# Performance work log

Hardware: AMD Instinct MI355X
Metric: run time of the kernel (lower is better)

Reference implementation:

```python
import jax, jax.numpy as jnp
import numpy as np

N = 500000      # examples = M * (nr+1)
K = 20          # context set size (indices[:, 3:])
NR = 24         # negatives per positive
H = 128         # hidden_channels == node feature dim
NODES = 10000   # ingredient vocabulary


def setup_inputs() -> dict:
    key = jax.random.key(0)
    ks = jax.random.split(key, 6)
    indices = jax.random.randint(ks[0], (N, 3 + K), 0, NODES)
    x = jax.random.normal(ks[1], (NODES, H), dtype=jnp.float32)
    scale = 0.02
    W1 = jax.random.normal(ks[2], (H, 3 * H), dtype=jnp.float32) * scale
    b1 = jnp.zeros((H,), jnp.float32)
    W2 = jax.random.normal(ks[3], (H // 2, H), dtype=jnp.float32) * scale
    b2 = jnp.zeros((H // 2,), jnp.float32)
    W3 = jax.random.normal(ks[4], (1, H // 2), dtype=jnp.float32) * scale
    b3 = jnp.zeros((1,), jnp.float32)
    return {"indices": indices, "nr": NR, "x": x,
            "W1": W1, "b1": b1, "W2": W2, "b2": b2, "W3": W3, "b3": b3}


def _embed_context(ctx_idx, x, nr):
    # ctx_idx: [N, K]; one context row per group of (nr+1) examples
    new_idx = ctx_idx[:-1:nr + 1]                 # [M, K]
    emb = x[new_idx]                               # [M, K, H] gather
    s = emb.sum(axis=1)                            # [M, H]
    norm = jnp.maximum((new_idx > 0).sum(axis=1), 1).astype(x.dtype)[:, None]
    mean = s / norm                                # masked mean over context
    return jnp.repeat(mean, nr + 1, axis=0)        # broadcast back to [N, H]


def reference(indices, nr, x, W1, b1, W2, b2, W3, b3):
    ing1 = x[indices[:, 0]]                        # [N, H]
    ing2 = x[indices[:, 1]]                        # [N, H]
    set_emb = _embed_context(indices[:, 3:], x, nr)  # [N, H]
    y = jnp.concatenate([ing1, ing2, set_emb], axis=1)  # [N, 3H]
    y = jax.nn.relu(y @ W1.T + b1)
    y = jax.nn.relu(y @ W2.T + b2)
    return y @ W3.T + b3                           # [N, 1]
```

## Files before the change

kernel.cpp:

```cpp
#include <hip/hip_runtime.h>
#include <hip/hip_bf16.h>

#define N_ROWS   500000
#define NR1      25
#define NGROUPS  20000
#define KCTX     20
#define H        128
#define NODES    10000
#define IDX_COLS 23

#define NT       4
#define RPB      (NT * 128)
#define MAXG     22

typedef __attribute__((ext_vector_type(8))) short short8;
typedef __attribute__((ext_vector_type(4))) float f32x4;

__device__ __forceinline__ unsigned pkbf(float lo, float hi) {
  __hip_bfloat162 h = __float22bfloat162_rn(make_float2(lo, hi));
  union { __hip_bfloat162 h; unsigned u; } c; c.h = h;
  return c.u;
}
__device__ __forceinline__ float bf2f(unsigned short u) {
  union { unsigned u; float f; } c; c.u = ((unsigned)u) << 16; return c.f;
}

#define PN 64
#define PRE_BLOCKS ((NODES + PN - 1) / PN)
__global__ __launch_bounds__(256) void k_precompute(
    const float* __restrict__ x, const float* __restrict__ W1,
    const int* __restrict__ indices,
    unsigned short* __restrict__ Pb, int2* __restrict__ idx2) {
  const int tid = threadIdx.x;
  const int m   = blockIdx.y;

  if (m == 3) {
    const int stride = PRE_BLOCKS * 256;
    for (int r = blockIdx.x * 256 + tid; r < N_ROWS; r += stride) {
      idx2[r] = make_int2(indices[(size_t)r * IDX_COLS + 0],
                          indices[(size_t)r * IDX_COLS + 1]);
    }
    return;
  }

  __shared__ short wlds[128][136];
  const int tbase = blockIdx.x * PN;

#pragma unroll
  for (int it = 0; it < 16; ++it) {
    const int f  = it * 256 + tid;
    const int j  = f >> 5;
    const int q4 = f & 31;
    const float4 v = *(const float4*)(W1 + (size_t)j * (3 * H) + m * H + q4 * 4);
    *(unsigned*)&wlds[j][q4 * 4]     = pkbf(v.x, v.y);
    *(unsigned*)&wlds[j][q4 * 4 + 2] = pkbf(v.z, v.w);
  }
  __syncthreads();

  const int lane = tid & 63;
  const int wv   = tid >> 6;
  const int col  = lane & 15;
  const int quad = lane >> 4;

  int node = tbase + wv * 16 + col;
  if (node > NODES - 1) node = NODES - 1;
  const float4* __restrict__ xr = (const float4*)(x + (size_t)node * H);

  short8 Af[4];
#pragma unroll
  for (int kt = 0; kt < 4; ++kt) {
    const int f4 = kt * 8 + quad * 2;
    const float4 v0 = xr[f4], v1 = xr[f4 + 1];
    union { short8 v; unsigned u[4]; } pk;
    pk.u[0] = pkbf(v0.x, v0.y);
    pk.u[1] = pkbf(v0.z, v0.w);
    pk.u[2] = pkbf(v1.x, v1.y);
    pk.u[3] = pkbf(v1.z, v1.w);
    Af[kt] = pk.v;
  }

  f32x4 acc[8];
#pragma unroll
  for (int ct = 0; ct < 8; ++ct) acc[ct] = (f32x4)(0.f);

#pragma unroll
  for (int kt = 0; kt < 4; ++kt) {
#pragma unroll
    for (int ct = 0; ct < 8; ++ct) {
      const short8 Bf = *(const short8*)&wlds[ct * 16 + col][kt * 32 + quad * 8];
      acc[ct] = __builtin_amdgcn_mfma_f32_16x16x32_bf16(Af[kt], Bf, acc[ct], 0, 0, 0);
    }
  }

  unsigned short* __restrict__ Pm = Pb + (size_t)m * NODES * H;
#pragma unroll
  for (int reg = 0; reg < 4; ++reg) {
    const int n = tbase + wv * 16 + quad * 4 + reg;
    if (n < NODES) {
#pragma unroll
      for (int ct = 0; ct < 8; ++ct) {
        union { unsigned u; unsigned short s[2]; } c;
        c.u = pkbf(acc[ct][reg], 0.f);
        Pm[(size_t)n * H + ct * 16 + col] = c.s[0];
      }
    }
  }
}

__global__ __launch_bounds__(256) void k_main(
    const int* __restrict__ indices, const int2* __restrict__ idx2,
    const unsigned short* __restrict__ P1b, const unsigned short* __restrict__ P2b,
    const unsigned short* __restrict__ P3b,
    const float* __restrict__ W2, const float* __restrict__ b1,
    const float* __restrict__ b2, const float* __restrict__ W3,
    const float* __restrict__ b3, float* __restrict__ out) {
  __shared__ short w2s[64][136];
  __shared__ float cgs[MAXG][132];

  const int tid   = threadIdx.x;
  const int rbase = blockIdx.x * RPB;
  const int gbase = rbase / NR1;

  for (int idx = tid; idx < 64 * 64; idx += 256) {
    const int n  = idx >> 6;
    const int kp = idx & 63;
    const float2 w = *(const float2*)(W2 + (size_t)n * H + kp * 2);
    *(unsigned*)&w2s[n][kp * 2] = pkbf(w.x, w.y);
  }

  {
    int rlast = rbase + RPB - 1; if (rlast > N_ROWS - 1) rlast = N_ROWS - 1;
    const int G   = rlast / NR1 - gbase + 1;
    const int jj  = (tid & 63) * 2;
    const int sub = tid >> 6;
    const float2 b1v = *(const float2*)(b1 + jj);
#pragma unroll
    for (int it = 0; it < 6; ++it) {
      const int gi = it * 4 + sub;
      if (gi < G) {
        const int* __restrict__ rowidx =
            indices + (size_t)(gbase + gi) * NR1 * IDX_COLS + 3;
        float s0 = 0.f, s1 = 0.f;
        int cnt = 0;
#pragma unroll
        for (int c = 0; c < KCTX; ++c) {
          const int idx = rowidx[c];
          const unsigned w = *(const unsigned*)(P3b + (size_t)idx * H + jj);
          s0 += bf2f((unsigned short)(w & 0xffffu));
          s1 += bf2f((unsigned short)(w >> 16));
          cnt += (idx > 0) ? 1 : 0;
        }
        const float rn = 1.f / (float)((cnt > 1) ? cnt : 1);
        cgs[gi][jj]     = b1v.x + s0 * rn;
        cgs[gi][jj + 1] = b1v.y + s1 * rn;
      }
    }
  }
  __syncthreads();

  const int lane = tid & 63;
  const int wv   = tid >> 6;
  const int col  = lane & 15;
  const int quad = lane >> 4;

  float b2v[4], w3v[4];
#pragma unroll
  for (int ct = 0; ct < 4; ++ct) {
    b2v[ct] = b2[ct * 16 + col];
    w3v[ct] = W3[ct * 16 + col];
  }
  const float bias3 = b3[0];

  short8 ua[2][2][4], ub[2][2][4];
  int    gl[2][2];

  {
    const int R = rbase + wv * 32;
#pragma unroll
    for (int rt = 0; rt < 2; ++rt) {
      const int r  = R + rt * 16 + col;
      const int rc = (r < N_ROWS) ? r : (N_ROWS - 1);
      const int2 ii = idx2[rc];
      const short8* __restrict__ pa = (const short8*)(P1b + (size_t)ii.x * H);
      const short8* __restrict__ pb = (const short8*)(P2b + (size_t)ii.y * H);
#pragma unroll
      for (int kt = 0; kt < 4; ++kt) {
        ua[0][rt][kt] = pa[kt * 4 + quad];
        ub[0][rt][kt] = pb[kt * 4 + quad];
      }
      gl[0][rt] = rc / NR1 - gbase;
    }
  }

#pragma unroll
  for (int t = 0; t < NT; ++t) {
    const int cur = t & 1;
    const int nxt = cur ^ 1;
    const int Rt  = rbase + t * 128 + wv * 32;

    short8 A[2][4];
#pragma unroll
    for (int rt = 0; rt < 2; ++rt) {
#pragma unroll
      for (int kt = 0; kt < 4; ++kt) {
        union { short8 v; unsigned short s[8]; } va, vb;
        va.v = ua[cur][rt][kt];
        vb.v = ub[cur][rt][kt];
        const float4 c0 = *(const float4*)&cgs[gl[cur][rt]][kt * 32 + quad * 8];
        const float4 c1 = *(const float4*)&cgs[gl[cur][rt]][kt * 32 + quad * 8 + 4];
        const float h0 = fmaxf(bf2f(va.s[0]) + bf2f(vb.s[0]) + c0.x, 0.f);
        const float h1 = fmaxf(bf2f(va.s[1]) + bf2f(vb.s[1]) + c0.y, 0.f);
        const float h2 = fmaxf(bf2f(va.s[2]) + bf2f(vb.s[2]) + c0.z, 0.f);
        const float h3 = fmaxf(bf2f(va.s[3]) + bf2f(vb.s[3]) + c0.w, 0.f);
        const float h4 = fmaxf(bf2f(va.s[4]) + bf2f(vb.s[4]) + c1.x, 0.f);
        const float h5 = fmaxf(bf2f(va.s[5]) + bf2f(vb.s[5]) + c1.y, 0.f);
        const float h6 = fmaxf(bf2f(va.s[6]) + bf2f(vb.s[6]) + c1.z, 0.f);
        const float h7 = fmaxf(bf2f(va.s[7]) + bf2f(vb.s[7]) + c1.w, 0.f);
        union { short8 v; unsigned u[4]; } pk;
        pk.u[0] = pkbf(h0, h1);
        pk.u[1] = pkbf(h2, h3);
        pk.u[2] = pkbf(h4, h5);
        pk.u[3] = pkbf(h6, h7);
        A[rt][kt] = pk.v;
      }
    }

    if (t + 1 < NT) {
      const int Rn = rbase + (t + 1) * 128 + wv * 32;
#pragma unroll
      for (int rt = 0; rt < 2; ++rt) {
        const int r  = Rn + rt * 16 + col;
        const int rc = (r < N_ROWS) ? r : (N_ROWS - 1);
        const int2 ii = idx2[rc];
        const short8* __restrict__ pa = (const short8*)(P1b + (size_t)ii.x * H);
        const short8* __restrict__ pb = (const short8*)(P2b + (size_t)ii.y * H);
#pragma unroll
        for (int kt = 0; kt < 4; ++kt) {
          ua[nxt][rt][kt] = pa[kt * 4 + quad];
          ub[nxt][rt][kt] = pb[kt * 4 + quad];
        }
        gl[nxt][rt] = rc / NR1 - gbase;
      }
    }

    f32x4 acc[2][4];
#pragma unroll
    for (int rt = 0; rt < 2; ++rt)
#pragma unroll
      for (int ct = 0; ct < 4; ++ct) acc[rt][ct] = (f32x4)(0.f);
#pragma unroll
    for (int kt = 0; kt < 4; ++kt) {
#pragma unroll
      for (int ct = 0; ct < 4; ++ct) {
        const short8 Bf = *(const short8*)&w2s[ct * 16 + col][kt * 32 + quad * 8];
#pragma unroll
        for (int rt = 0; rt < 2; ++rt)
          acc[rt][ct] = __builtin_amdgcn_mfma_f32_16x16x32_bf16(
              A[rt][kt], Bf, acc[rt][ct], 0, 0, 0);
      }
    }
#pragma unroll
    for (int rt = 0; rt < 2; ++rt) {
#pragma unroll
      for (int reg = 0; reg < 4; ++reg) {
        float s = 0.f;
#pragma unroll
        for (int ct = 0; ct < 4; ++ct)
          s += fmaxf(acc[rt][ct][reg] + b2v[ct], 0.f) * w3v[ct];
        s += __shfl_xor(s, 1);
        s += __shfl_xor(s, 2);
        s += __shfl_xor(s, 4);
        s += __shfl_xor(s, 8);
        if (col == 0) {
          const int row = Rt + rt * 16 + quad * 4 + reg;
          if (row < N_ROWS) out[row] = s + bias3;
        }
      }
    }
  }
}

extern "C" void kernel_launch(void* const* d_in, const int* in_sizes, int n_in,
                              void* d_out, int out_size, void* d_ws, size_t ws_size,
                              hipStream_t stream) {
  const int*   indices = (const int*)  d_in[0];
  const float* x  = (const float*)d_in[2];
  const float* W1 = (const float*)d_in[3];
  const float* b1 = (const float*)d_in[4];
  const float* W2 = (const float*)d_in[5];
  const float* b2 = (const float*)d_in[6];
  const float* W3 = (const float*)d_in[7];
  const float* b3 = (const float*)d_in[8];
  float* out = (float*)d_out;

  unsigned short* Pb  = (unsigned short*)d_ws;
  unsigned short* P1b = Pb;
  unsigned short* P2b = Pb + (size_t)NODES * H;
  unsigned short* P3b = Pb + (size_t)2 * NODES * H;
  int2* idx2 = (int2*)(Pb + (size_t)3 * NODES * H);

  dim3 gpre(PRE_BLOCKS, 4);
  k_precompute<<<gpre, 256, 0, stream>>>(x, W1, indices, Pb, idx2);
  k_main<<<(N_ROWS + RPB - 1) / RPB, 256, 0, stream>>>(indices, idx2,
                                                       P1b, P2b, P3b,
                                                       W2, b1, b2, W3, b3, out);
}
```

Before: 158.4 us.

## Process 128 rows per block and issue gathers before shared setup

Each block now handles a single 128-row tile instead of four, which removes the in-block double-buffered prefetch loop and launches four times as many blocks. The gathers of the first-layer partial rows are issued at the very start of the kernel, so their latency overlaps the W2 staging and the context-group reduction into shared memory. The cost is that every block repeats the W2 conversion to shared memory, and each block has fewer groups to amortise the context sums over, so redundant context work at tile boundaries goes up.

Measured after the change: 170.1 us. 7.4% more time.

```diff
diff --git a/kernel.cpp b/kernel.cpp
--- a/kernel.cpp
+++ b/kernel.cpp
@@ -9,9 +9,8 @@
 #define NODES    10000
 #define IDX_COLS 23
 
-#define NT       4
-#define RPB      (NT * 128)
-#define MAXG     22
+#define RPB      128
+#define MAXG     7
 
 typedef __attribute__((ext_vector_type(8))) short short8;
 typedef __attribute__((ext_vector_type(4))) float f32x4;
@@ -121,6 +120,31 @@
   const int rbase = blockIdx.x * RPB;
   const int gbase = rbase / NR1;
 
+  const int lane = tid & 63;
+  const int wv   = tid >> 6;
+  const int col  = lane & 15;
+  const int quad = lane >> 4;
+
+  short8 ua[2][4], ub[2][4];
+  int    gl[2];
+  {
+    const int R = rbase + wv * 32;
+#pragma unroll
+    for (int rt = 0; rt < 2; ++rt) {
+      const int r  = R + rt * 16 + col;
+      const int rc = (r < N_ROWS) ? r : (N_ROWS - 1);
+      const int2 ii = idx2[rc];
+      const short8* __restrict__ pa = (const short8*)(P1b + (size_t)ii.x * H);
+      const short8* __restrict__ pb = (const short8*)(P2b + (size_t)ii.y * H);
+#pragma unroll
+      for (int kt = 0; kt < 4; ++kt) {
+        ua[rt][kt] = pa[kt * 4 + quad];
+        ub[rt][kt] = pb[kt * 4 + quad];
+      }
+      gl[rt] = rc / NR1 - gbase;
+    }
+  }
+
   for (int idx = tid; idx < 64 * 64; idx += 256) {
     const int n  = idx >> 6;
     const int kp = idx & 63;
@@ -135,7 +159,7 @@
     const int sub = tid >> 6;
     const float2 b1v = *(const float2*)(b1 + jj);
 #pragma unroll
-    for (int it = 0; it < 6; ++it) {
+    for (int it = 0; it < 2; ++it) {
       const int gi = it * 4 + sub;
       if (gi < G) {
         const int* __restrict__ rowidx =
@@ -158,11 +182,6 @@
   }
   __syncthreads();
 
-  const int lane = tid & 63;
-  const int wv   = tid >> 6;
-  const int col  = lane & 15;
-  const int quad = lane >> 4;
-
   float b2v[4], w3v[4];
 #pragma unroll
   for (int ct = 0; ct < 4; ++ct) {
@@ -171,110 +190,66 @@
   }
   const float bias3 = b3[0];
 
-  short8 ua[2][2][4], ub[2][2][4];
-  int    gl[2][2];
-
-  {
-    const int R = rbase + wv * 32;
-#pragma unroll
-    for (int rt = 0; rt < 2; ++rt) {
-      const int r  = R + rt * 16 + col;
-      const int rc = (r < N_ROWS) ? r : (N_ROWS - 1);
-      const int2 ii = idx2[rc];
-      const short8* __restrict__ pa = (const short8*)(P1b + (size_t)ii.x * H);
-      const short8* __restrict__ pb = (const short8*)(P2b + (size_t)ii.y * H);
-#pragma unroll
-      for (int kt = 0; kt < 4; ++kt) {
-        ua[0][rt][kt] = pa[kt * 4 + quad];
-        ub[0][rt][kt] = pb[kt * 4 + quad];
-      }
-      gl[0][rt] = rc / NR1 - gbase;
-    }
-  }
-
-#pragma unroll
-  for (int t = 0; t < NT; ++t) {
-    const int cur = t & 1;
-    const int nxt = cur ^ 1;
-    const int Rt  = rbase + t * 128 + wv * 32;
-
-    short8 A[2][4];
-#pragma unroll
-    for (int rt = 0; rt < 2; ++rt) {
-#pragma unroll
-      for (int kt = 0; kt < 4; ++kt) {
-        union { short8 v; unsigned short s[8]; } va, vb;
-        va.v = ua[cur][rt][kt];
-        vb.v = ub[cur][rt][kt];
-        const float4 c0 = *(const float4*)&cgs[gl[cur][rt]][kt * 32 + quad * 8];
-        const float4 c1 = *(const float4*)&cgs[gl[cur][rt]][kt * 32 + quad * 8 + 4];
-        const float h0 = fmaxf(bf2f(va.s[0]) + bf2f(vb.s[0]) + c0.x, 0.f);
-        const float h1 = fmaxf(bf2f(va.s[1]) + bf2f(vb.s[1]) + c0.y, 0.f);
-        const float h2 = fmaxf(bf2f(va.s[2]) + bf2f(vb.s[2]) + c0.z, 0.f);
-        const float h3 = fmaxf(bf2f(va.s[3]) + bf2f(vb.s[3]) + c0.w, 0.f);
-        const float h4 = fmaxf(bf2f(va.s[4]) + bf2f(vb.s[4]) + c1.x, 0.f);
-        const float h5 = fmaxf(bf2f(va.s[5]) + bf2f(vb.s[5]) + c1.y, 0.f);
-        const float h6 = fmaxf(bf2f(va.s[6]) + bf2f(vb.s[6]) + c1.z, 0.f);
-        const float h7 = fmaxf(bf2f(va.s[7]) + bf2f(vb.s[7]) + c1.w, 0.f);
-        union { short8 v; unsigned u[4]; } pk;
-        pk.u[0] = pkbf(h0, h1);
-        pk.u[1] = pkbf(h2, h3);
-        pk.u[2] = pkbf(h4, h5);
-        pk.u[3] = pkbf(h6, h7);
-        A[rt][kt] = pk.v;
-      }
-    }
-
-    if (t + 1 < NT) {
-      const int Rn = rbase + (t + 1) * 128 + wv * 32;
-#pragma unroll
-      for (int rt = 0; rt < 2; ++rt) {
-        const int r  = Rn + rt * 16 + col;
-        const int rc = (r < N_ROWS) ? r : (N_ROWS - 1);
-        const int2 ii = idx2[rc];
-        const short8* __restrict__ pa = (const short8*)(P1b + (size_t)ii.x * H);
-        const short8* __restrict__ pb = (const short8*)(P2b + (size_t)ii.y * H);
-#pragma unroll
-        for (int kt = 0; kt < 4; ++kt) {
-          ua[nxt][rt][kt] = pa[kt * 4 + quad];
-          ub[nxt][rt][kt] = pb[kt * 4 + quad];
-        }
-        gl[nxt][rt] = rc / NR1 - gbase;
-      }
-    }
-
-    f32x4 acc[2][4];
-#pragma unroll
-    for (int rt = 0; rt < 2; ++rt)
-#pragma unroll
-      for (int ct = 0; ct < 4; ++ct) acc[rt][ct] = (f32x4)(0.f);
+  short8 A[2][4];
+#pragma unroll
+  for (int rt = 0; rt < 2; ++rt) {
 #pragma unroll
     for (int kt = 0; kt < 4; ++kt) {
-#pragma unroll
-      for (int ct = 0; ct < 4; ++ct) {
-        const short8 Bf = *(const short8*)&w2s[ct * 16 + col][kt * 32 + quad * 8];
-#pragma unroll
-        for (int rt = 0; rt < 2; ++rt)
-          acc[rt][ct] = __builtin_amdgcn_mfma_f32_16x16x32_bf16(
-              A[rt][kt], Bf, acc[rt][ct], 0, 0, 0);
-      }
-    }
-#pragma unroll
-    for (int rt = 0; rt < 2; ++rt) {
-#pragma unroll
-      for (int reg = 0; reg < 4; ++reg) {
-        float s = 0.f;
-#pragma unroll
-        for (int ct = 0; ct < 4; ++ct)
-          s += fmaxf(acc[rt][ct][reg] + b2v[ct], 0.f) * w3v[ct];
-        s += __shfl_xor(s, 1);
-        s += __shfl_xor(s, 2);
-        s += __shfl_xor(s, 4);
-        s += __shfl_xor(s, 8);
-        if (col == 0) {
-          const int row = Rt + rt * 16 + quad * 4 + reg;
-          if (row < N_ROWS) out[row] = s + bias3;
-        }
+      union { short8 v; unsigned short s[8]; } va, vb;
+      va.v = ua[rt][kt];
+      vb.v = ub[rt][kt];
+      const float4 c0 = *(const float4*)&cgs[gl[rt]][kt * 32 + quad * 8];
+      const float4 c1 = *(const float4*)&cgs[gl[rt]][kt * 32 + quad * 8 + 4];
+      const float h0 = fmaxf(bf2f(va.s[0]) + bf2f(vb.s[0]) + c0.x, 0.f);
+      const float h1 = fmaxf(bf2f(va.s[1]) + bf2f(vb.s[1]) + c0.y, 0.f);
+      const float h2 = fmaxf(bf2f(va.s[2]) + bf2f(vb.s[2]) + c0.z, 0.f);
+      const float h3 = fmaxf(bf2f(va.s[3]) + bf2f(vb.s[3]) + c0.w, 0.f);
+      const float h4 = fmaxf(bf2f(va.s[4]) + bf2f(vb.s[4]) + c1.x, 0.f);
+      const float h5 = fmaxf(bf2f(va.s[5]) + bf2f(vb.s[5]) + c1.y, 0.f);
+      const float h6 = fmaxf(bf2f(va.s[6]) + bf2f(vb.s[6]) + c1.z, 0.f);
+      const float h7 = fmaxf(bf2f(va.s[7]) + bf2f(vb.s[7]) + c1.w, 0.f);
+      union { short8 v; unsigned u[4]; } pk;
+      pk.u[0] = pkbf(h0, h1);
+      pk.u[1] = pkbf(h2, h3);
+      pk.u[2] = pkbf(h4, h5);
+      pk.u[3] = pkbf(h6, h7);
+      A[rt][kt] = pk.v;
+    }
+  }
+
+  f32x4 acc[2][4];
+#pragma unroll
+  for (int rt = 0; rt < 2; ++rt)
+#pragma unroll
+    for (int ct = 0; ct < 4; ++ct) acc[rt][ct] = (f32x4)(0.f);
+#pragma unroll
+  for (int kt = 0; kt < 4; ++kt) {
+#pragma unroll
+    for (int ct = 0; ct < 4; ++ct) {
+      const short8 Bf = *(const short8*)&w2s[ct * 16 + col][kt * 32 + quad * 8];
+#pragma unroll
+      for (int rt = 0; rt < 2; ++rt)
+        acc[rt][ct] = __builtin_amdgcn_mfma_f32_16x16x32_bf16(
+            A[rt][kt], Bf, acc[rt][ct], 0, 0, 0);
+    }
+  }
+
+  const int Rt = rbase + wv * 32;
+#pragma unroll
+  for (int rt = 0; rt < 2; ++rt) {
+#pragma unroll
+    for (int reg = 0; reg < 4; ++reg) {
+      float s = 0.f;
+#pragma unroll
+      for (int ct = 0; ct < 4; ++ct)
+        s += fmaxf(acc[rt][ct][reg] + b2v[ct], 0.f) * w3v[ct];
+      s += __shfl_xor(s, 1);
+      s += __shfl_xor(s, 2);
+      s += __shfl_xor(s, 4);
+      s += __shfl_xor(s, 8);
+      if (col == 0) {
+        const int row = Rt + rt * 16 + quad * 4 + reg;
+        if (row < N_ROWS) out[row] = s + bias3;
       }
     }
   }
```
